# Performance work log

Measured on AMD Instinct MI355X. Metric: run time of the kernel, lower is better.

Reference implementation:

```python
import jax, jax.numpy as jnp
import numpy as np
import math

B, S, HID, H = 8, 512, 1024, 16
D = HID // H
ATT_SPAN = 512  # max_position_embeddings


def setup_inputs() -> dict:
    key = jax.random.key(0)
    ks = jax.random.split(key, 12)
    sd = 0.02
    hidden_states = jax.random.normal(ks[0], (B, S, HID), jnp.float32)
    attention_mask = jnp.zeros((B, 1, 1, S), jnp.float32)
    # DeBERTa build_relative_position: rel[i, j] = i - j, shape [1, 1, S, S]
    rel = (jnp.arange(S)[:, None] - jnp.arange(S)[None, :]).astype(jnp.int32)
    relative_pos = rel[None, None]
    Wq = jax.random.normal(ks[1], (HID, HID), jnp.float32) * sd
    bq = jnp.zeros((HID,), jnp.float32)
    Wk = jax.random.normal(ks[2], (HID, HID), jnp.float32) * sd
    bk = jnp.zeros((HID,), jnp.float32)
    Wv = jax.random.normal(ks[3], (HID, HID), jnp.float32) * sd
    bv = jnp.zeros((HID,), jnp.float32)
    Wpk = jax.random.normal(ks[4], (HID, HID), jnp.float32) * sd
    bpk = jnp.zeros((HID,), jnp.float32)
    rel_emb = jax.random.normal(ks[5], (2 * ATT_SPAN, HID), jnp.float32) * sd
    return dict(hidden_states=hidden_states, attention_mask=attention_mask,
                relative_pos=relative_pos, Wq=Wq, bq=bq, Wk=Wk, bk=bk,
                Wv=Wv, bv=bv, Wpk=Wpk, bpk=bpk, rel_emb=rel_emb)


def _fwd(hidden_states, attention_mask, relative_pos, Wq, bq, Wk, bk, Wv, bv, Wpk, bpk, rel_emb):
    b, s, _ = hidden_states.shape

    def proj(x, W, bias):  # [b,s,hid] -> [b,h,s,d]
        return (x @ W.T + bias).reshape(b, s, H, D).transpose(0, 2, 1, 3)

    q = proj(hidden_states, Wq, bq)
    k = proj(hidden_states, Wk, bk)
    v = proj(hidden_states, Wv, bv)

    # content-to-content scores, scaled by sqrt(3*num_heads) as in source
    s_content = jnp.einsum('bhid,bhjd->bhij', q, k) / math.sqrt(3.0 * H)

    # positional projections (source uses pos_key layer for BOTH key and query)
    # rel_emb: [2*ATT_SPAN, HID] -> [H, 2*ATT_SPAN, D]
    pos = (rel_emb @ Wpk.T + bpk).reshape(2 * ATT_SPAN, H, D).transpose(1, 0, 2)

    # c2p: q @ pos^T / sqrt(all_head_size * 3), then gather along last axis
    c2p_full = jnp.einsum('bhid,hpd->bhip', q, pos) / math.sqrt(HID * 3.0)  # [b,h,s,2P]
    c2p_pos = jnp.clip(relative_pos + ATT_SPAN, 0, 2 * ATT_SPAN - 1)
    c2p_pos = jnp.broadcast_to(c2p_pos, (b, H, s, s)).astype(jnp.int32)
    c2p = jnp.take_along_axis(c2p_full, c2p_pos, axis=-1)  # [b,h,s,s]

    # p2c: pos / sqrt(3*H) @ k^T, gather along dim -2 with same index
    p2c_full = jnp.einsum('hpd,bhjd->bhpj', pos / math.sqrt(3.0 * H), k)  # [b,h,2P,s]
    p2c = jnp.take_along_axis(p2c_full, c2p_pos, axis=-2)  # [b,h,s,s]

    score = s_content + c2p + p2c + attention_mask
    probs = jax.nn.softmax(score, axis=-1)  # dropout is identity in eval
    out = jnp.einsum('bhij,bhjd->bhid', probs, v)
    return out.transpose(0, 2, 1, 3).reshape(b, s, HID)


def reference(hidden_states, attention_mask, relative_pos, Wq, bq, Wk, bk, Wv, bv, Wpk, bpk, rel_emb):
    return _fwd(hidden_states, attention_mask, relative_pos, Wq, bq, Wk, bk, Wv, bv, Wpk, bpk, rel_emb)
```

## Files before the change

### kernel.cpp

```cpp
#include <hip/hip_runtime.h>
#include <cstdint>
#include <cstddef>

static constexpr int NB  = 8;
static constexpr int S   = 512;
static constexpr int HID = 1024;
static constexpr int NH  = 16;
static constexpr int DH  = 64;
static constexpr int P2  = 1024;

static constexpr float INV_S1 = 0.14433756729740643f;

typedef __bf16 v8bf  __attribute__((ext_vector_type(8)));
typedef __bf16 v4bf  __attribute__((ext_vector_type(4)));
typedef float  f32x4 __attribute__((ext_vector_type(4)));

#define MFMA16(acc, a, b) acc = __builtin_amdgcn_mfma_f32_16x16x32_bf16(a, b, acc, 0, 0, 0)

__global__ void castall(const float* __restrict__ x,  const float* __restrict__ wq,
                        const float* __restrict__ wk, const float* __restrict__ wv,
                        const float* __restrict__ wpk, const float* __restrict__ rel,
                        __bf16* __restrict__ ob) {
  size_t e = ((size_t)blockIdx.x * 256 + threadIdx.x) * 4;
  if (e >= 9437184) return;
  const float* src; size_t off;
  if (e < 4194304) { src = x; off = e; }
  else {
    int r = (int)((e - 4194304) >> 20);
    off = (e - 4194304) & 1048575;
    src = (r == 0) ? wq : (r == 1) ? wk : (r == 2) ? wv : (r == 3) ? wpk : rel;
  }
  float4 v = *(const float4*)(src + off);
  v4bf o;
  o[0] = (__bf16)v.x; o[1] = (__bf16)v.y; o[2] = (__bf16)v.z; o[3] = (__bf16)v.w;
  *(v4bf*)(ob + e) = o;
}

__launch_bounds__(256, 4)
__global__ void proj_gemm(const __bf16* __restrict__ Xb, const __bf16* __restrict__ Rb,
                          const __bf16* __restrict__ Wqb, const __bf16* __restrict__ Wkb,
                          const __bf16* __restrict__ Wvb, const __bf16* __restrict__ Wpkb,
                          const float* __restrict__ bq, const float* __restrict__ bk_,
                          const float* __restrict__ bv_, const float* __restrict__ bpk,
                          __bf16* __restrict__ qo, __bf16* __restrict__ ko,
                          __bf16* __restrict__ vto, __bf16* __restrict__ po) {
  const int z = blockIdx.z;
  const __bf16* A; const __bf16* W; const float* bias; __bf16* out; int M; float osc;
  if      (z == 0) { A = Xb; W = Wqb;  bias = bq;  out = qo;  M = 4096; osc = INV_S1; }
  else if (z == 1) { A = Xb; W = Wkb;  bias = bk_; out = ko;  M = 4096; osc = 1.0f; }
  else if (z == 2) { A = Xb; W = Wvb;  bias = bv_; out = vto; M = 4096; osc = 1.0f; }
  else             { A = Rb; W = Wpkb; bias = bpk; out = po;  M = 1024; osc = INV_S1; }
  const int m0 = blockIdx.x * 128;
  if (m0 >= M) return;
  const int n0 = blockIdx.y * 128;
  const int K = 1024;

  __shared__ __bf16 Al[128 * 72];
  __shared__ __bf16 Bl[128 * 72];

  const int t = threadIdx.x;
  const int w = t >> 6, lane = t & 63, q4 = lane >> 4, cc = lane & 15;
  const int wm = w >> 1, wn = w & 1;
  const int srow = t >> 1, sseg = (t & 1) * 32;

  f32x4 acc[4][4] = {};

  for (int k0 = 0; k0 < K; k0 += 64) {
    __syncthreads();
    {
      const __bf16* ga = &A[(size_t)(m0 + srow) * K + k0 + sseg];
      const __bf16* gb = &W[(size_t)(n0 + srow) * K + k0 + sseg];
      int4 a0 = *(const int4*)ga,        a1 = *(const int4*)(ga + 8);
      int4 a2 = *(const int4*)(ga + 16), a3 = *(const int4*)(ga + 24);
      int4 b0 = *(const int4*)gb,        b1 = *(const int4*)(gb + 8);
      int4 b2 = *(const int4*)(gb + 16), b3 = *(const int4*)(gb + 24);
      *(int4*)(&Al[srow * 72 + sseg])      = a0;
      *(int4*)(&Al[srow * 72 + sseg + 8])  = a1;
      *(int4*)(&Al[srow * 72 + sseg + 16]) = a2;
      *(int4*)(&Al[srow * 72 + sseg + 24]) = a3;
      *(int4*)(&Bl[srow * 72 + sseg])      = b0;
      *(int4*)(&Bl[srow * 72 + sseg + 8])  = b1;
      *(int4*)(&Bl[srow * 72 + sseg + 16]) = b2;
      *(int4*)(&Bl[srow * 72 + sseg + 24]) = b3;
    }
    __syncthreads();
    #pragma unroll
    for (int kk = 0; kk < 2; kk++) {
      v8bf af[4], bfg[4];
      #pragma unroll
      for (int mt = 0; mt < 4; mt++)
        af[mt] = *(const v8bf*)(&Al[(wm * 64 + mt * 16 + cc) * 72 + kk * 32 + q4 * 8]);
      #pragma unroll
      for (int nt = 0; nt < 4; nt++)
        bfg[nt] = *(const v8bf*)(&Bl[(wn * 64 + nt * 16 + cc) * 72 + kk * 32 + q4 * 8]);
      #pragma unroll
      for (int mt = 0; mt < 4; mt++)
        #pragma unroll
        for (int nt = 0; nt < 4; nt++)
          MFMA16(acc[mt][nt], af[mt], bfg[nt]);
    }
  }

  #pragma unroll
  for (int mt = 0; mt < 4; mt++) {
    #pragma unroll
    for (int nt = 0; nt < 4; nt++) {
      int n = n0 + wn * 64 + nt * 16 + cc;
      float bsv = bias[n];
      if (z == 2) {
        int m_base = m0 + wm * 64 + mt * 16 + q4 * 4;
        int bb = m_base >> 9, ss = m_base & 511, hh = n >> 6, dd = n & 63;
        v4bf st;
        st[0] = (__bf16)(acc[mt][nt][0] + bsv);
        st[1] = (__bf16)(acc[mt][nt][1] + bsv);
        st[2] = (__bf16)(acc[mt][nt][2] + bsv);
        st[3] = (__bf16)(acc[mt][nt][3] + bsv);
        *(v4bf*)(&out[(((size_t)bb * 16 + hh) * 64 + dd) * 512 + ss]) = st;
      } else {
        #pragma unroll
        for (int r = 0; r < 4; r++) {
          int m = m0 + wm * 64 + mt * 16 + q4 * 4 + r;
          float val = (acc[mt][nt][r] + bsv) * osc;
          size_t idx;
          if (z < 2)
            idx = ((size_t)(m >> 9) * 16 + (n >> 6)) * (512 * 64) + (size_t)(m & 511) * 64 + (n & 63);
          else
            idx = (size_t)(n >> 6) * (1024 * 64) + (size_t)m * 64 + (n & 63);
          out[idx] = (__bf16)val;
        }
      }
    }
  }
}

__launch_bounds__(512, 4)
__global__ void attn(const __bf16* __restrict__ qb, const __bf16* __restrict__ kb,
                     const __bf16* __restrict__ vtb, const __bf16* __restrict__ posb,
                     const float* __restrict__ mask, float* __restrict__ out) {
  const int bh = blockIdx.y, b = bh >> 4, h = bh & 15;
  const int i0 = blockIdx.x * 128;

  __shared__ __bf16 Sb[128 * 152];
  __shared__ __bf16 Prl[128 * 72];

  const int t = threadIdx.x, w = t >> 6, lane = t & 63, q4 = lane >> 4, cc = lane & 15;
  const int arow = w * 16;
  const size_t bho = (size_t)bh * (S * DH);
  const __bf16* qp  = qb  + bho;
  const __bf16* kp  = kb  + bho;
  const __bf16* vtp = vtb + bho;
  const __bf16* pp  = posb + (size_t)h * (P2 * DH);

  v8bf aq0 = *(const v8bf*)(&qp[(size_t)(i0 + arow + cc) * DH + q4 * 8]);
  v8bf aq1 = *(const v8bf*)(&qp[(size_t)(i0 + arow + cc) * DH + 32 + q4 * 8]);

  f32x4 Oc[4] = {};
  float mrow[4], lrow[4];
  #pragma unroll
  for (int r = 0; r < 4; r++) { mrow[r] = -__builtin_inff(); lrow[r] = 0.f; }

#define LDP(d0, d1, U) { int p_ = pw0 + 16 * (U) + cc; p_ = min(max(p_, 0), P2 - 1); \
  const __bf16* pr_ = &pp[(size_t)p_ * DH + q4 * 8]; \
  d0 = *(const v8bf*)pr_; d1 = *(const v8bf*)(pr_ + 32); }
#define LDK(d0, d1, NT) { const __bf16* kr_ = &kp[(size_t)(j0 + (NT) * 16 + cc) * DH + q4 * 8]; \
  d0 = *(const v8bf*)kr_; d1 = *(const v8bf*)(kr_ + 32); }
#define GT(U, P0, P1) { f32x4 g_ = {}; MFMA16(g_, aq0, P0); MFMA16(g_, aq1, P1); \
  _Pragma("unroll") for (int r_ = 0; r_ < 4; r_++) { \
    int jj_ = q4 * 4 + r_ - 16 * (U) - cc + 63; \
    if ((unsigned)jj_ < 64u) Sb[(arow + q4 * 4 + r_) * 152 + jj_ * 2] = (__bf16)(g_[r_] * 0.8660254f); } }
#define HT(U, NT, P0, P1, K0, K1) { f32x4 h_ = {}; MFMA16(h_, P0, K0); MFMA16(h_, P1, K1); \
  _Pragma("unroll") for (int r_ = 0; r_ < 4; r_++) { \
    int ar_ = 16 * (U) + q4 * 4 + r_ + 16 * (NT) + cc - 63; \
    if ((unsigned)ar_ < 16u) Sb[(arow + ar_) * 152 + (16 * (NT) + cc) * 2 + 1] = (__bf16)h_[r_]; } }
#define CT(NT, K0, K1) { f32x4 c_ = {}; MFMA16(c_, aq0, K0); MFMA16(c_, aq1, K1); accc[NT] = c_; }

  for (int jt = 0; jt < 8; jt++) {
    const int j0 = jt * 64;
    const int pw0 = i0 + arow - j0 + 449;

    float mk[4];
    #pragma unroll
    for (int nt = 0; nt < 4; nt++) mk[nt] = mask[(size_t)b * S + j0 + nt * 16 + cc];

    f32x4 accc[4];
    v8bf p40,p41,p30,p31,p20,p21,p10,p11,p00,p01;
    v8bf k00,k01,k10,k11,k20,k21,k30,k31;

    LDP(p40, p41, 4); LDK(k00, k01, 0);
    LDP(p30, p31, 3); LDK(k10, k11, 1);
    GT(4, p40, p41); HT(4, 0, p40, p41, k00, k01); CT(0, k00, k01);
    LDP(p20, p21, 2); LDK(k20, k21, 2);
    GT(3, p30, p31); HT(3, 0, p30, p31, k00, k01); HT(3, 1, p30, p31, k10, k11); CT(1, k10, k11);
    LDP(p10, p11, 1); LDK(k30, k31, 3);
    GT(2, p20, p21); HT(2, 1, p20, p21, k10, k11); HT(2, 2, p20, p21, k20, k21); CT(2, k20, k21);
    LDP(p00, p01, 0);
    GT(1, p10, p11); HT(1, 2, p10, p11, k20, k21); HT(1, 3, p10, p11, k30, k31); CT(3, k30, k31);
    GT(0, p00, p01); HT(0, 3, p00, p01, k30, k31);

    float sc[4][4];
    float tmax[4] = { -__builtin_inff(), -__builtin_inff(), -__builtin_inff(), -__builtin_inff() };
    #pragma unroll
    for (int nt = 0; nt < 4; nt++) {
      int jj = nt * 16 + cc;
      #pragma unroll
      for (int r = 0; r < 4; r++) {
        const __bf16* slot = &Sb[(arow + q4 * 4 + r) * 152 + jj * 2];
        float s = accc[nt][r] + (float)slot[0] + (float)slot[1] + mk[nt];
        sc[nt][r] = s;
        tmax[r] = fmaxf(tmax[r], s);
      }
    }
    #pragma unroll
    for (int off = 1; off < 16; off <<= 1)
      #pragma unroll
      for (int r = 0; r < 4; r++) tmax[r] = fmaxf(tmax[r], __shfl_xor(tmax[r], off, 64));

    v8bf vf[2][4];
    #pragma unroll
    for (int kk = 0; kk < 2; kk++)
      #pragma unroll
      for (int dt = 0; dt < 4; dt++)
        vf[kk][dt] = *(const v8bf*)(&vtp[(size_t)(dt * 16 + cc) * S + j0 + kk * 32 + q4 * 8]);

    float alpha[4], psum[4];
    #pragma unroll
    for (int r = 0; r < 4; r++) {
      float mnew = fmaxf(mrow[r], tmax[r]);
      alpha[r] = __expf(mrow[r] - mnew);
      mrow[r] = mnew;
      psum[r] = 0.f;
    }
    #pragma unroll
    for (int nt = 0; nt < 4; nt++)
      #pragma unroll
      for (int r = 0; r < 4; r++) {
        float p = __expf(sc[nt][r] - mrow[r]);
        psum[r] += p;
        Prl[(arow + q4 * 4 + r) * 72 + nt * 16 + cc] = (__bf16)p;
      }
    #pragma unroll
    for (int off = 1; off < 16; off <<= 1)
      #pragma unroll
      for (int r = 0; r < 4; r++) psum[r] += __shfl_xor(psum[r], off, 64);
    #pragma unroll
    for (int r = 0; r < 4; r++) lrow[r] = lrow[r] * alpha[r] + psum[r];
    #pragma unroll
    for (int dt = 0; dt < 4; dt++)
      #pragma unroll
      for (int r = 0; r < 4; r++) Oc[dt][r] *= alpha[r];

    #pragma unroll
    for (int kk = 0; kk < 2; kk++) {
      v8bf ap = *(const v8bf*)(&Prl[(arow + cc) * 72 + kk * 32 + q4 * 8]);
      #pragma unroll
      for (int dt = 0; dt < 4; dt++)
        MFMA16(Oc[dt], ap, vf[kk][dt]);
    }
  }

  #pragma unroll
  for (int r = 0; r < 4; r++) {
    float rl = 1.0f / lrow[r];
    #pragma unroll
    for (int dt = 0; dt < 4; dt++) {
      int i = i0 + arow + q4 * 4 + r;
      int d = dt * 16 + cc;
      out[((size_t)b * S + i) * HID + h * 64 + d] = Oc[dt][r] * rl;
    }
  }
#undef LDP
#undef LDK
#undef GT
#undef HT
#undef CT
}

extern "C" void kernel_launch(void* const* d_in, const int* in_sizes, int n_in,
                              void* d_out, int out_size, void* d_ws, size_t ws_size,
                              hipStream_t stream) {
  const float* hs   = (const float*)d_in[0];
  const float* mask = (const float*)d_in[1];
  const float* Wq  = (const float*)d_in[3];
  const float* bq  = (const float*)d_in[4];
  const float* Wk  = (const float*)d_in[5];
  const float* bk  = (const float*)d_in[6];
  const float* Wv  = (const float*)d_in[7];
  const float* bv  = (const float*)d_in[8];
  const float* Wpk = (const float*)d_in[9];
  const float* bpk = (const float*)d_in[10];
  const float* rel = (const float*)d_in[11];
  float* out = (float*)d_out;

  char* ws = (char*)d_ws;
  __bf16* cb   = (__bf16*)ws;
  __bf16* Xb   = cb;
  __bf16* Wqb  = cb + 4194304;
  __bf16* Wkb  = cb + 5242880;
  __bf16* Wvb  = cb + 6291456;
  __bf16* Wpkb = cb + 7340032;
  __bf16* Rb   = cb + 8388608;
  __bf16* qb   = (__bf16*)(ws + 18874368);
  __bf16* kb   = (__bf16*)(ws + 27262976);
  __bf16* vtb  = (__bf16*)(ws + 35651584);
  __bf16* posb = (__bf16*)(ws + 44040192);

  castall<<<9216, 256, 0, stream>>>(hs, Wq, Wk, Wv, Wpk, rel, cb);

  proj_gemm<<<dim3(32, 8, 4), 256, 0, stream>>>(Xb, Rb, Wqb, Wkb, Wvb, Wpkb,
                                                bq, bk, bv, bpk, qb, kb, vtb, posb);

  attn<<<dim3(4, 128), 512, 0, stream>>>(qb, kb, vtb, posb, mask, out);
}
```

Before: 264.5 us.

## Use direct global-to-LDS loads with swizzle in projection GEMM; shrink attention LDS

In the projection GEMM, the register-staged global→LDS tile copy is replaced with `global_load_lds` 16-byte direct transfers. The LDS layout becomes an unpadded, XOR-swizzled one, and the fragment reads are adjusted to match; this is meant to avoid register round-trips and bank conflicts. In the attention kernel, the separate probability buffer is folded into the score scratch buffer, which is shrunk to a tighter stride. The launch-bounds occupancy hint is raised from 4 to 8 to allow more resident blocks. The higher occupancy target may cap registers per thread and cause spills in the register-heavy attention loop.

```diff
diff --git a/kernel.cpp b/kernel.cpp
--- a/kernel.cpp
+++ b/kernel.cpp
@@ -16,6 +16,10 @@
 typedef float  f32x4 __attribute__((ext_vector_type(4)));
 
 #define MFMA16(acc, a, b) acc = __builtin_amdgcn_mfma_f32_16x16x32_bf16(a, b, acc, 0, 0, 0)
+
+#define GLOAD_LDS16(gp, lp) __builtin_amdgcn_global_load_lds( \
+    (const __attribute__((address_space(1))) void*)(gp), \
+    (__attribute__((address_space(3))) void*)(lp), 16, 0, 0)
 
 __global__ void castall(const float* __restrict__ x,  const float* __restrict__ wq,
                         const float* __restrict__ wk, const float* __restrict__ wv,
@@ -55,44 +59,37 @@
   const int n0 = blockIdx.y * 128;
   const int K = 1024;
 
-  __shared__ __bf16 Al[128 * 72];
-  __shared__ __bf16 Bl[128 * 72];
+  __shared__ __bf16 Al[128 * 64];
+  __shared__ __bf16 Bl[128 * 64];
 
   const int t = threadIdx.x;
   const int w = t >> 6, lane = t & 63, q4 = lane >> 4, cc = lane & 15;
   const int wm = w >> 1, wn = w & 1;
-  const int srow = t >> 1, sseg = (t & 1) * 32;
+  const int srow_in = lane >> 3;
+  const int sseg    = ((lane & 7) ^ srow_in) * 8;
 
   f32x4 acc[4][4] = {};
 
   for (int k0 = 0; k0 < K; k0 += 64) {
     __syncthreads();
-    {
-      const __bf16* ga = &A[(size_t)(m0 + srow) * K + k0 + sseg];
-      const __bf16* gb = &W[(size_t)(n0 + srow) * K + k0 + sseg];
-      int4 a0 = *(const int4*)ga,        a1 = *(const int4*)(ga + 8);
-      int4 a2 = *(const int4*)(ga + 16), a3 = *(const int4*)(ga + 24);
-      int4 b0 = *(const int4*)gb,        b1 = *(const int4*)(gb + 8);
-      int4 b2 = *(const int4*)(gb + 16), b3 = *(const int4*)(gb + 24);
-      *(int4*)(&Al[srow * 72 + sseg])      = a0;
-      *(int4*)(&Al[srow * 72 + sseg + 8])  = a1;
-      *(int4*)(&Al[srow * 72 + sseg + 16]) = a2;
-      *(int4*)(&Al[srow * 72 + sseg + 24]) = a3;
-      *(int4*)(&Bl[srow * 72 + sseg])      = b0;
-      *(int4*)(&Bl[srow * 72 + sseg + 8])  = b1;
-      *(int4*)(&Bl[srow * 72 + sseg + 16]) = b2;
-      *(int4*)(&Bl[srow * 72 + sseg + 24]) = b3;
+    #pragma unroll
+    for (int i = 0; i < 4; i++) {
+      int rr = w * 32 + i * 8;
+      int gr = rr + srow_in;
+      GLOAD_LDS16(&A[(size_t)(m0 + gr) * K + k0 + sseg], &Al[rr * 64]);
+      GLOAD_LDS16(&W[(size_t)(n0 + gr) * K + k0 + sseg], &Bl[rr * 64]);
     }
     __syncthreads();
     #pragma unroll
     for (int kk = 0; kk < 2; kk++) {
       v8bf af[4], bfg[4];
+      const int phys = ((4 * kk + q4) ^ (cc & 7)) * 8;
       #pragma unroll
       for (int mt = 0; mt < 4; mt++)
-        af[mt] = *(const v8bf*)(&Al[(wm * 64 + mt * 16 + cc) * 72 + kk * 32 + q4 * 8]);
+        af[mt] = *(const v8bf*)(&Al[(wm * 64 + mt * 16 + cc) * 64 + phys]);
       #pragma unroll
       for (int nt = 0; nt < 4; nt++)
-        bfg[nt] = *(const v8bf*)(&Bl[(wn * 64 + nt * 16 + cc) * 72 + kk * 32 + q4 * 8]);
+        bfg[nt] = *(const v8bf*)(&Bl[(wn * 64 + nt * 16 + cc) * 64 + phys]);
       #pragma unroll
       for (int mt = 0; mt < 4; mt++)
         #pragma unroll
@@ -133,15 +130,14 @@
   }
 }
 
-__launch_bounds__(512, 4)
+__launch_bounds__(512, 8)
 __global__ void attn(const __bf16* __restrict__ qb, const __bf16* __restrict__ kb,
                      const __bf16* __restrict__ vtb, const __bf16* __restrict__ posb,
                      const float* __restrict__ mask, float* __restrict__ out) {
   const int bh = blockIdx.y, b = bh >> 4, h = bh & 15;
   const int i0 = blockIdx.x * 128;
 
-  __shared__ __bf16 Sb[128 * 152];
-  __shared__ __bf16 Prl[128 * 72];
+  __shared__ __bf16 Sb[128 * 136];
 
   const int t = threadIdx.x, w = t >> 6, lane = t & 63, q4 = lane >> 4, cc = lane & 15;
   const int arow = w * 16;
@@ -167,11 +163,11 @@
 #define GT(U, P0, P1) { f32x4 g_ = {}; MFMA16(g_, aq0, P0); MFMA16(g_, aq1, P1); \
   _Pragma("unroll") for (int r_ = 0; r_ < 4; r_++) { \
     int jj_ = q4 * 4 + r_ - 16 * (U) - cc + 63; \
-    if ((unsigned)jj_ < 64u) Sb[(arow + q4 * 4 + r_) * 152 + jj_ * 2] = (__bf16)(g_[r_] * 0.8660254f); } }
+    if ((unsigned)jj_ < 64u) Sb[(arow + q4 * 4 + r_) * 136 + jj_ * 2] = (__bf16)(g_[r_] * 0.8660254f); } }
 #define HT(U, NT, P0, P1, K0, K1) { f32x4 h_ = {}; MFMA16(h_, P0, K0); MFMA16(h_, P1, K1); \
   _Pragma("unroll") for (int r_ = 0; r_ < 4; r_++) { \
     int ar_ = 16 * (U) + q4 * 4 + r_ + 16 * (NT) + cc - 63; \
-    if ((unsigned)ar_ < 16u) Sb[(arow + ar_) * 152 + (16 * (NT) + cc) * 2 + 1] = (__bf16)h_[r_]; } }
+    if ((unsigned)ar_ < 16u) Sb[(arow + ar_) * 136 + (16 * (NT) + cc) * 2 + 1] = (__bf16)h_[r_]; } }
 #define CT(NT, K0, K1) { f32x4 c_ = {}; MFMA16(c_, aq0, K0); MFMA16(c_, aq1, K1); accc[NT] = c_; }
 
   for (int jt = 0; jt < 8; jt++) {
@@ -204,7 +200,7 @@
       int jj = nt * 16 + cc;
       #pragma unroll
       for (int r = 0; r < 4; r++) {
-        const __bf16* slot = &Sb[(arow + q4 * 4 + r) * 152 + jj * 2];
+        const __bf16* slot = &Sb[(arow + q4 * 4 + r) * 136 + jj * 2];
         float s = accc[nt][r] + (float)slot[0] + (float)slot[1] + mk[nt];
         sc[nt][r] = s;
         tmax[r] = fmaxf(tmax[r], s);
@@ -236,7 +232,7 @@
       for (int r = 0; r < 4; r++) {
         float p = __expf(sc[nt][r] - mrow[r]);
         psum[r] += p;
-        Prl[(arow + q4 * 4 + r) * 72 + nt * 16 + cc] = (__bf16)p;
+        Sb[(arow + q4 * 4 + r) * 136 + nt * 16 + cc] = (__bf16)p;
       }
     #pragma unroll
     for (int off = 1; off < 16; off <<= 1)
@@ -251,7 +247,7 @@
 
     #pragma unroll
     for (int kk = 0; kk < 2; kk++) {
-      v8bf ap = *(const v8bf*)(&Prl[(arow + cc) * 72 + kk * 32 + q4 * 8]);
+      v8bf ap = *(const v8bf*)(&Sb[(arow + cc) * 136 + kk * 32 + q4 * 8]);
       #pragma unroll
       for (int dt = 0; dt < 4; dt++)
         MFMA16(Oc[dt], ap, vf[kk][dt]);
```

New measurement: 421.3 us. 1.59x slower.
